# Kernel tuning notes

Measured on AMD Instinct MI355X. Metric: run time of the kernel, lower is better.

## Reference

```python
import jax, jax.numpy as jnp
import numpy as np

NEG_SLOPE = 0.2  # PyG GATv2Conv default negative_slope
EPS_BN = 1e-5


def gatv2(x, src, dst, ea, Wl, bl, Wr, br, We, att, bias, heads, C):
    """GATv2Conv (PyG semantics, eval mode / no dropout).
    x: [N, Fin]; src/dst: [Et] (self-loops already appended); ea: [Et, edge_dim].
    Returns (out [N, heads*C], alpha [Et, heads])."""
    N = x.shape[0]
    xl = (x @ Wl + bl).reshape(N, heads, C)   # lin_l -> source features
    xr = (x @ Wr + br).reshape(N, heads, C)   # lin_r -> target features
    e = (ea @ We).reshape(-1, heads, C)       # lin_edge (no bias in PyG)
    m = jax.nn.leaky_relu(xl[src] + xr[dst] + e, NEG_SLOPE)  # [Et, H, C]
    logit = jnp.einsum('ehc,hc->eh', m, att)                  # [Et, H]
    # segment softmax over destination node
    amax = jax.ops.segment_max(logit, dst, num_segments=N)
    expv = jnp.exp(logit - amax[dst])
    denom = jax.ops.segment_sum(expv, dst, num_segments=N)
    alpha = expv / (denom[dst] + 1e-16)
    out = jax.ops.segment_sum(xl[src] * alpha[:, :, None], dst, num_segments=N)
    return out.reshape(N, heads * C) + bias, alpha


def setup_inputs() -> dict:
    key = jax.random.key(0)
    ks = list(jax.random.split(key, 20))
    N, E, H, C = 100000, 1600000, 2, 32
    D = H * C  # 64
    def nrm(i, shape, s=0.1):
        return jax.random.normal(ks[i], shape, jnp.float32) * s
    return {
        'x': jax.random.normal(ks[0], (N, 2), jnp.float32),
        'edge_index': jax.random.randint(ks[1], (2, E), 0, N, dtype=jnp.int32),
        'edge_attr': jax.random.uniform(ks[2], (E, 1), dtype=jnp.float32),
        'Wl1': nrm(3, (2, D)), 'bl1': jnp.zeros((D,), jnp.float32),
        'Wr1': nrm(4, (2, D)), 'br1': jnp.zeros((D,), jnp.float32),
        'We1': nrm(5, (1, D)), 'att1': nrm(6, (H, C)), 'bias1': jnp.zeros((D,), jnp.float32),
        'skip_W': nrm(7, (2, D)), 'skip_b': jnp.zeros((D,), jnp.float32),
        'bn_gamma': jnp.ones((D,), jnp.float32), 'bn_beta': jnp.zeros((D,), jnp.float32),
        'Wl2': nrm(8, (D, C)), 'bl2': jnp.zeros((C,), jnp.float32),
        'Wr2': nrm(9, (D, C)), 'br2': jnp.zeros((C,), jnp.float32),
        'We2': nrm(10, (1, C)), 'att2': nrm(11, (1, C)), 'bias2': jnp.zeros((C,), jnp.float32),
        'Wc1': nrm(12, (C, C)), 'bc1': jnp.zeros((C,), jnp.float32),
        'Wc2': nrm(13, (C, 10)), 'bc2': jnp.zeros((10,), jnp.float32),
        'Wt1': nrm(14, (C, C)), 'bt1': jnp.zeros((C,), jnp.float32),
        'Wt2': nrm(15, (C, 20)), 'bt2': jnp.zeros((20,), jnp.float32),
    }


def reference(x, edge_index, edge_attr, Wl1, bl1, Wr1, br1, We1, att1, bias1,
              skip_W, skip_b, bn_gamma, bn_beta,
              Wl2, bl2, Wr2, br2, We2, att2, bias2,
              Wc1, bc1, Wc2, bc2, Wt1, bt1, Wt2, bt2):
    N = x.shape[0]
    src0, dst0 = edge_index[0], edge_index[1]
    # add_self_loops with fill_value='mean': self-loop attr = mean of incoming edge attrs per node
    loop = jnp.arange(N, dtype=edge_index.dtype)
    deg = jax.ops.segment_sum(jnp.ones(src0.shape, jnp.float32), dst0, num_segments=N)
    loop_attr = jax.ops.segment_sum(edge_attr, dst0, num_segments=N) / jnp.maximum(deg, 1.0)[:, None]
    src = jnp.concatenate([src0, loop])
    dst = jnp.concatenate([dst0, loop])
    ea = jnp.concatenate([edge_attr, loop_attr], axis=0)

    h, _ = gatv2(x, src, dst, ea, Wl1, bl1, Wr1, br1, We1, att1, bias1, heads=2, C=32)
    h = h + x @ skip_W + skip_b
    # BatchNorm1d, training-style batch statistics (deterministic)
    mu = h.mean(0)
    var = h.var(0)
    h = (h - mu) / jnp.sqrt(var + EPS_BN) * bn_gamma + bn_beta
    h = jax.nn.elu(h)
    h, alpha = gatv2(h, src, dst, ea, Wl2, bl2, Wr2, br2, We2, att2, bias2, heads=1, C=32)
    h = jax.nn.elu(h)
    h_type = jax.nn.relu(h @ Wt1 + bt1)
    h_clone = jax.nn.relu(h @ Wc1 + bc1)
    h_type = jax.nn.log_softmax(h_type @ Wt2 + bt2, axis=1)
    h_clone = jax.nn.log_softmax(h_clone @ Wc2 + bc2, axis=1)
    out = jnp.concatenate([h_clone, h_type], axis=1)  # [N, 30]
    return out, alpha
```

## Files before the change

### kernel.cpp

```cpp
#include <hip/hip_runtime.h>
#include <math.h>

#define NEG_SLOPE 0.2f
#define CNT_SHIFT 44
#define EA_SCALE 262144.0f
#define EA_INV (1.0f / 262144.0f)

typedef float f2 __attribute__((ext_vector_type(2)));
__device__ __forceinline__ f2 max2(f2 a, f2 b) { return __builtin_elementwise_max(a, b); }
__device__ __forceinline__ f2 lrelu2(f2 m) { return max2(m, m * NEG_SLOPE); }

__device__ __forceinline__ float lrelu(float x) { return fmaxf(x, NEG_SLOPE * x); }
__device__ __forceinline__ float elu1(float x) { return x > 0.f ? x : __expf(x) - 1.f; }

__global__ void k0p(const int* __restrict__ dst, const float* __restrict__ ea,
                    unsigned long long* __restrict__ packed,
                    unsigned short* __restrict__ rankA, int E) {
    int t = blockIdx.x * blockDim.x + threadIdx.x;
    if (t >= E) return;
    int d = dst[t];
    unsigned long long inc = (1ULL << CNT_SHIFT)
                           | (unsigned long long)__float2uint_rn(ea[t] * EA_SCALE);
    unsigned long long old = atomicAdd(&packed[d], inc);
    rankA[t] = (unsigned short)(old >> CNT_SHIFT);
}

__global__ void kscanA(const unsigned long long* __restrict__ packed,
                       int* __restrict__ rowstart, int* __restrict__ bsum,
                       int* __restrict__ cntA, float* __restrict__ asumA, int N) {
    __shared__ int sm[256];
    int t = threadIdx.x;
    int i = blockIdx.x * 256 + t;
    int v = 0;
    if (i < N) {
        unsigned long long p = packed[i];
        int c = (int)(p >> CNT_SHIFT);
        cntA[i] = c;
        asumA[i] = (float)(p & ((1ULL << CNT_SHIFT) - 1)) * EA_INV;
        v = c + 1;
    }
    sm[t] = v;
    __syncthreads();
    for (int off = 1; off < 256; off <<= 1) {
        int u = (t >= off) ? sm[t - off] : 0;
        __syncthreads();
        sm[t] += u;
        __syncthreads();
    }
    if (i < N) rowstart[i] = sm[t] - v;
    if (t == 255) bsum[blockIdx.x] = sm[255];
}

__global__ void kscanB(int* __restrict__ bsum, int B) {
    __shared__ int sm[512];
    int t = threadIdx.x;
    int v = (t < B) ? bsum[t] : 0;
    sm[t] = v;
    __syncthreads();
    for (int off = 1; off < 512; off <<= 1) {
        int u = (t >= off) ? sm[t - off] : 0;
        __syncthreads();
        sm[t] += u;
        __syncthreads();
    }
    if (t < B) bsum[t] = sm[t] - v;
}

__global__ void kscanC(int* __restrict__ rowstart, const int* __restrict__ bsum, int N) {
    int i = blockIdx.x * blockDim.x + threadIdx.x;
    if (i < N) rowstart[i] += bsum[i >> 8];
}

__global__ void kscatter(const int* __restrict__ srcA, const int* __restrict__ dstA,
                         const float* __restrict__ ea, const float* __restrict__ asumA,
                         const int* __restrict__ cntA, const int* __restrict__ rowstart,
                         const unsigned short* __restrict__ rankA,
                         int2* __restrict__ edge2, int* __restrict__ posA, int E, int Et) {
    int t = blockIdx.x * blockDim.x + threadIdx.x;
    if (t >= Et) return;
    if (t < E) {
        int d = dstA[t];
        int r = min((int)rankA[t], cntA[d] - 1);
        int pos = rowstart[d] + r;
        edge2[pos] = make_int2(srcA[t], __float_as_int(ea[t]));
        posA[t] = pos;
    } else {
        int d = t - E;
        int cd = cntA[d];
        int pos = rowstart[d] + cd;
        float eav = asumA[d] / fmaxf((float)cd, 1.0f);
        edge2[pos] = make_int2(d, __float_as_int(eav));
    }
}

__global__ void __launch_bounds__(256, 4)
kL1(const float* __restrict__ x, const int2* __restrict__ edge2,
    const int* __restrict__ rowst, const int* __restrict__ cntA,
    const float* __restrict__ Wl, const float* __restrict__ bl,
    const float* __restrict__ Wr, const float* __restrict__ br,
    const float* __restrict__ We, const float* __restrict__ att,
    float* __restrict__ dstat, int N) {
    int wid = blockIdx.x * 4 + (threadIdx.x >> 6);
    int TW = gridDim.x * 4;
    int lane = threadIdx.x & 63;
    int h = lane >> 5, lane5 = lane & 31;
    int slot = lane5 >> 3, cl = lane5 & 7;
    int dc = h * 32 + cl * 4;

    float4 t4;
    t4 = *(const float4*)(Wl + dc);        f2 wl0a = {t4.x, t4.y}, wl0b = {t4.z, t4.w};
    t4 = *(const float4*)(Wl + 64 + dc);   f2 wl1a = {t4.x, t4.y}, wl1b = {t4.z, t4.w};
    t4 = *(const float4*)(We + dc);        f2 weva = {t4.x, t4.y}, wevb = {t4.z, t4.w};
    t4 = *(const float4*)(att + dc);       f2 atva = {t4.x, t4.y}, atvb = {t4.z, t4.w};
    t4 = *(const float4*)(Wr + dc);        f2 wr0a = {t4.x, t4.y}, wr0b = {t4.z, t4.w};
    t4 = *(const float4*)(Wr + 64 + dc);   f2 wr1a = {t4.x, t4.y}, wr1b = {t4.z, t4.w};
    t4 = *(const float4*)(bl + dc);        f2 bba  = {t4.x, t4.y}, bbb  = {t4.z, t4.w};
    t4 = *(const float4*)(br + dc);        bba += (f2){t4.x, t4.y}; bbb += (f2){t4.z, t4.w};

    for (int n = wid; n < N; n += TW) {
        float2 xd = ((const float2*)x)[n];
        f2 dsta = bba + xd.x * wr0a + xd.y * wr1a;
        f2 dstb = bbb + xd.x * wr0b + xd.y * wr1b;
        int start = rowst[n], len = cntA[n] + 1;
        float pd = 0.f, pa = 0.f, pb = 0.f;
        for (int base = 0; base < len; base += 8) {
            int iA = base + slot, iB = base + 4 + slot;
            bool aA = iA < len, aB = iB < len;
            int2 eA = edge2[start + (aA ? iA : len - 1)];
            int2 eB = edge2[start + (aB ? iB : len - 1)];
            float2 xsA = ((const float2*)x)[eA.x];
            float2 xsB = ((const float2*)x)[eB.x];
            float evA = __int_as_float(eA.y), evB = __int_as_float(eB.y);
            f2 mAa = dsta + xsA.x * wl0a + xsA.y * wl1a + evA * weva;
            f2 mAb = dstb + xsA.x * wl0b + xsA.y * wl1b + evA * wevb;
            f2 mBa = dsta + xsB.x * wl0a + xsB.y * wl1a + evB * weva;
            f2 mBb = dstb + xsB.x * wl0b + xsB.y * wl1b + evB * wevb;
            f2 psA = lrelu2(mAa) * atva + lrelu2(mAb) * atvb;
            f2 psB = lrelu2(mBa) * atva + lrelu2(mBb) * atvb;
            float pA = psA.x + psA.y;
            float pB = psB.x + psB.y;
            pA += __shfl_xor(pA, 1); pB += __shfl_xor(pB, 1);
            pA += __shfl_xor(pA, 2); pB += __shfl_xor(pB, 2);
            pA += __shfl_xor(pA, 4); pB += __shfl_xor(pB, 4);
            float eevA = aA ? __expf(pA) : 0.f;
            float eevB = aB ? __expf(pB) : 0.f;
            pd += eevA + eevB;
            pa += eevA * xsA.x + eevB * xsB.x;
            pb += eevA * xsA.y + eevB * xsB.y;
        }
        pd += __shfl_xor(pd, 8);  pa += __shfl_xor(pa, 8);  pb += __shfl_xor(pb, 8);
        pd += __shfl_xor(pd, 16); pa += __shfl_xor(pa, 16); pb += __shfl_xor(pb, 16);
        if (lane5 == 0) {
            dstat[(size_t)n * 6 + h]     = pd;
            dstat[(size_t)n * 6 + 2 + h] = pa;
            dstat[(size_t)n * 6 + 4 + h] = pb;
        }
    }
}

__global__ void k3a(const float* __restrict__ x, const float* __restrict__ dstat,
                    const float* __restrict__ Wl, const float* __restrict__ bl,
                    const float* __restrict__ bias1,
                    const float* __restrict__ skW, const float* __restrict__ skb,
                    float* __restrict__ hout, float* __restrict__ partial, int N) {
    __shared__ float sv[256], sq[256];
    size_t total = (size_t)N * 64;
    size_t stride = (size_t)gridDim.x * blockDim.x;
    float s = 0.f, q = 0.f;
    for (size_t idx = (size_t)blockIdx.x * blockDim.x + threadIdx.x; idx < total; idx += stride) {
        int n = (int)(idx >> 6), d = (int)(idx & 63), h2 = d >> 5;
        const float* ps = &dstat[(size_t)n * 6];
        float den = ps[h2], t0 = ps[2 + h2], t1 = ps[4 + h2];
        float agg = t0 * Wl[d] + t1 * Wl[64 + d] + den * bl[d];
        float hv = agg / (den + 1e-16f) + bias1[d]
                 + x[2 * n] * skW[d] + x[2 * n + 1] * skW[64 + d] + skb[d];
        hout[idx] = hv;
        s += hv; q += hv * hv;
    }
    sv[threadIdx.x] = s; sq[threadIdx.x] = q;
    __syncthreads();
    if (threadIdx.x < 64) {
        float a = sv[threadIdx.x] + sv[threadIdx.x + 64] + sv[threadIdx.x + 128] + sv[threadIdx.x + 192];
        float b = sq[threadIdx.x] + sq[threadIdx.x + 64] + sq[threadIdx.x + 128] + sq[threadIdx.x + 192];
        partial[(size_t)blockIdx.x * 128 + threadIdx.x] = a;
        partial[(size_t)blockIdx.x * 128 + 64 + threadIdx.x] = b;
    }
}

__global__ void kred(const float* __restrict__ partial, float* __restrict__ mu,
                     float* __restrict__ rstd, int G, int N) {
    __shared__ float s1[256], s2[256];
    int c = blockIdx.x;
    float a = 0.f, b = 0.f;
    for (int i = threadIdx.x; i < G; i += blockDim.x) {
        a += partial[(size_t)i * 128 + c];
        b += partial[(size_t)i * 128 + 64 + c];
    }
    s1[threadIdx.x] = a; s2[threadIdx.x] = b;
    __syncthreads();
    for (int off = 128; off >= 1; off >>= 1) {
        if (threadIdx.x < off) {
            s1[threadIdx.x] += s1[threadIdx.x + off];
            s2[threadIdx.x] += s2[threadIdx.x + off];
        }
        __syncthreads();
    }
    if (threadIdx.x == 0) {
        float m = s1[0] / (float)N;
        float v = s2[0] / (float)N - m * m;
        mu[c] = m;
        rstd[c] = rsqrtf(v + 1e-5f);
    }
}

__global__ void k3c(const float* __restrict__ h, const float* __restrict__ mu,
                    const float* __restrict__ rstd, const float* __restrict__ gamma,
                    const float* __restrict__ beta,
                    const float* __restrict__ Wl, const float* __restrict__ bl,
                    const float* __restrict__ Wr, const float* __restrict__ br,
                    float* __restrict__ xl2, float* __restrict__ xr2, int N) {
    __shared__ float sh[4][64];
    int w = threadIdx.x >> 6, lane = threadIdx.x & 63;
    int n = blockIdx.x * 4 + w;
    bool valid = (n < N);
    if (valid) {
        float hv = h[(size_t)n * 64 + lane];
        hv = (hv - mu[lane]) * rstd[lane] * gamma[lane] + beta[lane];
        sh[w][lane] = elu1(hv);
    }
    __syncthreads();
    if (!valid) return;
    int c = lane & 31;
    const float* W = (lane < 32) ? Wl : Wr;
    const float* b = (lane < 32) ? bl : br;
    float acc = b[c];
    #pragma unroll
    for (int k = 0; k < 64; ++k) acc += sh[w][k] * W[k * 32 + c];
    ((lane < 32) ? xl2 : xr2)[(size_t)n * 32 + c] = acc;
}

__global__ void __launch_bounds__(256, 4)
kL2(const float* __restrict__ xl2, const float* __restrict__ xr2,
    const int2* __restrict__ edge2,
    const int* __restrict__ rowst, const int* __restrict__ cntA,
    const float* __restrict__ We, const float* __restrict__ att,
    float* __restrict__ evS, float* __restrict__ h2,
    float* __restrict__ denom2, int N) {
    int g = blockIdx.x * blockDim.x + threadIdx.x;
    int n = g >> 5;
    if (n >= N) return;
    int lane = g & 31;
    int slot = lane >> 3, cl = lane & 7;
    int c4 = cl * 4;
    float4 t4;
    t4 = *(const float4*)(We + c4);                      f2 weva = {t4.x, t4.y}, wevb = {t4.z, t4.w};
    t4 = *(const float4*)(att + c4);                     f2 atva = {t4.x, t4.y}, atvb = {t4.z, t4.w};
    t4 = *(const float4*)(xr2 + (size_t)n * 32 + c4);    f2 xrva = {t4.x, t4.y}, xrvb = {t4.z, t4.w};
    int start = rowst[n], len = cntA[n] + 1;
    float den = 0.f;
    f2 acca = {0.f, 0.f}, accb = {0.f, 0.f};

    for (int base = 0; base < len; base += 8) {
        int iA = base + slot, iB = base + 4 + slot;
        bool aA = iA < len, aB = iB < len;
        int2 eA = edge2[start + (aA ? iA : 0)];
        int2 eB = edge2[start + (aB ? iB : 0)];
        float4 xA4 = *(const float4*)(xl2 + (size_t)eA.x * 32 + c4);
        float4 xB4 = *(const float4*)(xl2 + (size_t)eB.x * 32 + c4);
        f2 xAa = {xA4.x, xA4.y}, xAb = {xA4.z, xA4.w};
        f2 xBa = {xB4.x, xB4.y}, xBb = {xB4.z, xB4.w};
        float evA = __int_as_float(eA.y), evB = __int_as_float(eB.y);
        f2 mAa = xAa + xrva + evA * weva;
        f2 mAb = xAb + xrvb + evA * wevb;
        f2 mBa = xBa + xrva + evB * weva;
        f2 mBb = xBb + xrvb + evB * wevb;
        f2 psA = lrelu2(mAa) * atva + lrelu2(mAb) * atvb;
        f2 psB = lrelu2(mBa) * atva + lrelu2(mBb) * atvb;
        float pA = psA.x + psA.y;
        float pB = psB.x + psB.y;
        pA += __shfl_xor(pA, 1); pB += __shfl_xor(pB, 1);
        pA += __shfl_xor(pA, 2); pB += __shfl_xor(pB, 2);
        pA += __shfl_xor(pA, 4); pB += __shfl_xor(pB, 4);
        float eevA = aA ? __expf(pA) : 0.f;
        float eevB = aB ? __expf(pB) : 0.f;
        if (cl == 0) {
            if (aA) evS[start + iA] = eevA;
            if (aB) evS[start + iB] = eevB;
        }
        den += eevA + eevB;
        acca += eevA * xAa + eevB * xBa;
        accb += eevA * xAb + eevB * xBb;
    }
    #pragma unroll
    for (int m = 8; m <= 16; m <<= 1) {
        den    += __shfl_xor(den, m);
        acca.x += __shfl_xor(acca.x, m);
        acca.y += __shfl_xor(acca.y, m);
        accb.x += __shfl_xor(accb.x, m);
        accb.y += __shfl_xor(accb.y, m);
    }
    float inv = 1.f / (den + 1e-16f);
    if (slot == 0) {
        float4 o = make_float4(acca.x * inv, acca.y * inv, accb.x * inv, accb.y * inv);
        *(float4*)(h2 + (size_t)n * 32 + c4) = o;
    }
    if (lane == 0) denom2[n] = den;
}

__global__ void k4c(const float* __restrict__ evS, const int* __restrict__ posA,
                    const int* __restrict__ dstA, const int* __restrict__ rowst,
                    const int* __restrict__ cntA, const float* __restrict__ denom,
                    float* __restrict__ alpha, int E, int Et) {
    int t = blockIdx.x * blockDim.x + threadIdx.x;
    if (t >= Et) return;
    float ev, den;
    if (t < E) {
        ev = evS[posA[t]];
        den = denom[dstA[t]];
    } else {
        int d = t - E;
        ev = evS[rowst[d] + cntA[d]];
        den = denom[d];
    }
    alpha[t] = ev / (den + 1e-16f);
}

__global__ void __launch_bounds__(256, 1)
k5(const float* __restrict__ h2, const float* __restrict__ bias2,
   const float* __restrict__ Wt1, const float* __restrict__ bt1,
   const float* __restrict__ Wt2, const float* __restrict__ bt2,
   const float* __restrict__ Wc1, const float* __restrict__ bc1,
   const float* __restrict__ Wc2, const float* __restrict__ bc2,
   float* __restrict__ out, int N) {
    __shared__ float sWt1[1024], sWc1[1024], sWt2[640], sWc2[320];
    __shared__ float sbt1[32], sbc1[32], sbt2[20], sbc2[10], sb2[32];
    for (int i = threadIdx.x; i < 1024; i += blockDim.x) { sWt1[i] = Wt1[i]; sWc1[i] = Wc1[i]; }
    for (int i = threadIdx.x; i < 640; i += blockDim.x) sWt2[i] = Wt2[i];
    for (int i = threadIdx.x; i < 320; i += blockDim.x) sWc2[i] = Wc2[i];
    if (threadIdx.x < 32) { sbt1[threadIdx.x] = bt1[threadIdx.x]; sbc1[threadIdx.x] = bc1[threadIdx.x]; sb2[threadIdx.x] = bias2[threadIdx.x]; }
    if (threadIdx.x < 20) sbt2[threadIdx.x] = bt2[threadIdx.x];
    if (threadIdx.x < 10) sbc2[threadIdx.x] = bc2[threadIdx.x];
    __syncthreads();
    int n = blockIdx.x * blockDim.x + threadIdx.x;
    if (n >= N) return;
    float h[32];
    #pragma unroll
    for (int k = 0; k < 32; ++k) h[k] = elu1(h2[(size_t)n * 32 + k] + sb2[k]);
    float lt[20], lc[10];
    #pragma unroll
    for (int o = 0; o < 20; ++o) lt[o] = sbt2[o];
    #pragma unroll
    for (int o = 0; o < 10; ++o) lc[o] = sbc2[o];
    #pragma unroll
    for (int j = 0; j < 32; ++j) {
        float at = sbt1[j], ac = sbc1[j];
        #pragma unroll
        for (int k = 0; k < 32; ++k) { at += h[k] * sWt1[k * 32 + j]; ac += h[k] * sWc1[k * 32 + j]; }
        float tj = fmaxf(at, 0.f), cj = fmaxf(ac, 0.f);
        #pragma unroll
        for (int o = 0; o < 20; ++o) lt[o] += tj * sWt2[j * 20 + o];
        #pragma unroll
        for (int o = 0; o < 10; ++o) lc[o] += cj * sWc2[j * 10 + o];
    }
    float mt = -1e30f, mc = -1e30f;
    #pragma unroll
    for (int o = 0; o < 20; ++o) mt = fmaxf(mt, lt[o]);
    #pragma unroll
    for (int o = 0; o < 10; ++o) mc = fmaxf(mc, lc[o]);
    float st = 0.f, sc = 0.f;
    #pragma unroll
    for (int o = 0; o < 20; ++o) st += __expf(lt[o] - mt);
    #pragma unroll
    for (int o = 0; o < 10; ++o) sc += __expf(lc[o] - mc);
    float lset = mt + __logf(st);
    float lsec = mc + __logf(sc);
    #pragma unroll
    for (int o = 0; o < 10; ++o) out[(size_t)n * 30 + o] = lc[o] - lsec;
    #pragma unroll
    for (int o = 0; o < 20; ++o) out[(size_t)n * 30 + 10 + o] = lt[o] - lset;
}

extern "C" void kernel_launch(void* const* d_in, const int* in_sizes, int n_in,
                              void* d_out, int out_size, void* d_ws, size_t ws_size,
                              hipStream_t stream) {
    const float* x     = (const float*)d_in[0];
    const int*   ei    = (const int*)d_in[1];
    const float* eattr = (const float*)d_in[2];
    const float* Wl1   = (const float*)d_in[3];
    const float* bl1   = (const float*)d_in[4];
    const float* Wr1   = (const float*)d_in[5];
    const float* br1   = (const float*)d_in[6];
    const float* We1   = (const float*)d_in[7];
    const float* att1  = (const float*)d_in[8];
    const float* bias1 = (const float*)d_in[9];
    const float* skW   = (const float*)d_in[10];
    const float* skb   = (const float*)d_in[11];
    const float* gamma = (const float*)d_in[12];
    const float* beta  = (const float*)d_in[13];
    const float* Wl2   = (const float*)d_in[14];
    const float* bl2   = (const float*)d_in[15];
    const float* Wr2   = (const float*)d_in[16];
    const float* br2   = (const float*)d_in[17];
    const float* We2   = (const float*)d_in[18];
    const float* att2  = (const float*)d_in[19];
    const float* bias2 = (const float*)d_in[20];
    const float* Wc1   = (const float*)d_in[21];
    const float* bc1   = (const float*)d_in[22];
    const float* Wc2   = (const float*)d_in[23];
    const float* bc2   = (const float*)d_in[24];
    const float* Wt1   = (const float*)d_in[25];
    const float* bt1   = (const float*)d_in[26];
    const float* Wt2   = (const float*)d_in[27];
    const float* bt2   = (const float*)d_in[28];

    const int N  = in_sizes[0] / 2;
    const int E  = in_sizes[1] / 2;
    const int Et = E + N;
    const int* srcA = ei;
    const int* dstA = ei + E;
    const int G3 = 1024;
    const int B  = (N + 255) / 256;

    char* p = (char*)d_ws;
    unsigned long long* packed = (unsigned long long*)p; p += (size_t)N * 8;
    int2*  edge2  = (int2*)p;  p += (size_t)Et * 8;
    int*   posA   = (int*)p;   p += (size_t)E * 4;
    unsigned short* rankA = (unsigned short*)p; p += (size_t)E * 2;
    float* hbuf   = (float*)p; p += (size_t)N * 64 * 4;
    float* xl2    = (float*)p; p += (size_t)N * 32 * 4;
    float* xr2    = (float*)p; p += (size_t)N * 32 * 4;
    float* evS    = (float*)p; p += (size_t)Et * 4;
    float* dstat  = (float*)p; p += (size_t)N * 6 * 4;
    int*   cntA   = (int*)p;   p += (size_t)N * 4;
    float* asumA  = (float*)p; p += (size_t)N * 4;
    int*   rowst  = (int*)p;   p += (size_t)N * 4;
    int*   bsum   = (int*)p;   p += 512 * 4;
    float* partial= (float*)p; p += (size_t)G3 * 128 * 4;
    float* mu     = (float*)p; p += 64 * 4;
    float* rstd   = (float*)p; p += 64 * 4;
    float* denom2 = (float*)p; p += (size_t)N * 4;
    float* h2     = hbuf;

    float* outMain  = (float*)d_out;
    float* outAlpha = outMain + (size_t)N * 30;

    hipMemsetAsync(packed, 0, (size_t)N * 8, stream);
    k0p<<<(E + 255) / 256, 256, 0, stream>>>(dstA, eattr, packed, rankA, E);
    kscanA<<<B, 256, 0, stream>>>(packed, rowst, bsum, cntA, asumA, N);
    kscanB<<<1, 512, 0, stream>>>(bsum, B);
    kscanC<<<B, 256, 0, stream>>>(rowst, bsum, N);
    kscatter<<<(Et + 255) / 256, 256, 0, stream>>>(srcA, dstA, eattr, asumA, cntA,
                                                   rowst, rankA, edge2, posA, E, Et);

    kL1<<<2048, 256, 0, stream>>>(x, edge2, rowst, cntA,
                                  Wl1, bl1, Wr1, br1, We1, att1, dstat, N);

    k3a<<<G3, 256, 0, stream>>>(x, dstat, Wl1, bl1, bias1, skW, skb, hbuf, partial, N);
    kred<<<64, 256, 0, stream>>>(partial, mu, rstd, G3, N);
    k3c<<<(N + 3) / 4, 256, 0, stream>>>(hbuf, mu, rstd, gamma, beta,
                                         Wl2, bl2, Wr2, br2, xl2, xr2, N);

    kL2<<<((size_t)N * 32 + 255) / 256, 256, 0, stream>>>(xl2, xr2, edge2, rowst, cntA,
                                                          We2, att2, evS, h2, denom2, N);
    k4c<<<(Et + 255) / 256, 256, 0, stream>>>(evS, posA, dstA, rowst, cntA, denom2,
                                              outAlpha, E, Et);

    k5<<<(N + 255) / 256, 256, 0, stream>>>(h2, bias2, Wt1, bt1, Wt2, bt2,
                                            Wc1, bc1, Wc2, bc2, outMain, N);
    (void)n_in; (void)out_size; (void)ws_size;
}
```

Before: 361.0 us.

## Compute layer-1 attention exps per edge in original order, scatter into CSR records

Layer-1 edge logits and their exponentials are now computed in the counting kernel, one thread per edge in coalesced original order, with no max subtraction, matching the old code. The results are scattered alongside the src/ea pair into a wider 32-byte CSR record. kL1 becomes a simple reduction over contiguous records, removing the random x gathers and the per-edge compute inside the per-node loop. The cost is a 4x larger edge record (more scatter bytes and a strided read in kL2), a per-edge 64-channel serial loop, and an evq buffer that overlaps hbuf.

```diff
diff --git a/kernel.cpp b/kernel.cpp
--- a/kernel.cpp
+++ b/kernel.cpp
@@ -13,16 +13,47 @@
 __device__ __forceinline__ float lrelu(float x) { return fmaxf(x, NEG_SLOPE * x); }
 __device__ __forceinline__ float elu1(float x) { return x > 0.f ? x : __expf(x) - 1.f; }
 
-__global__ void k0p(const int* __restrict__ dst, const float* __restrict__ ea,
+
+__global__ void k0p(const int* __restrict__ srcA, const int* __restrict__ dstA,
+                    const float* __restrict__ ea, const float* __restrict__ x,
+                    const float* __restrict__ Wl, const float* __restrict__ bl,
+                    const float* __restrict__ Wr, const float* __restrict__ br,
+                    const float* __restrict__ We, const float* __restrict__ att,
                     unsigned long long* __restrict__ packed,
-                    unsigned short* __restrict__ rankA, int E) {
+                    unsigned short* __restrict__ rankA,
+                    float4* __restrict__ evq, int E) {
+    __shared__ float sW[7][64];
+    if (threadIdx.x < 64) {
+        int d = threadIdx.x;
+        sW[0][d] = Wl[d];  sW[1][d] = Wl[64 + d];
+        sW[2][d] = We[d];  sW[3][d] = att[d];
+        sW[4][d] = Wr[d];  sW[5][d] = Wr[64 + d];
+        sW[6][d] = bl[d] + br[d];
+    }
+    __syncthreads();
     int t = blockIdx.x * blockDim.x + threadIdx.x;
     if (t >= E) return;
-    int d = dst[t];
+    int d = dstA[t], s = srcA[t];
+    float eav = ea[t];
     unsigned long long inc = (1ULL << CNT_SHIFT)
-                           | (unsigned long long)__float2uint_rn(ea[t] * EA_SCALE);
+                           | (unsigned long long)__float2uint_rn(eav * EA_SCALE);
     unsigned long long old = atomicAdd(&packed[d], inc);
     rankA[t] = (unsigned short)(old >> CNT_SHIFT);
+
+    float2 xs = ((const float2*)x)[s];
+    float2 xd = ((const float2*)x)[d];
+    float l0 = 0.f, l1 = 0.f;
+    #pragma unroll
+    for (int c = 0; c < 32; ++c) {
+        float m0 = xd.x * sW[4][c] + xd.y * sW[5][c] + sW[6][c]
+                 + xs.x * sW[0][c] + xs.y * sW[1][c] + eav * sW[2][c];
+        l0 += lrelu(m0) * sW[3][c];
+        int c2 = c + 32;
+        float m1 = xd.x * sW[4][c2] + xd.y * sW[5][c2] + sW[6][c2]
+                 + xs.x * sW[0][c2] + xs.y * sW[1][c2] + eav * sW[2][c2];
+        l1 += lrelu(m1) * sW[3][c2];
+    }
+    evq[t] = make_float4(__expf(l0), __expf(l1), xs.x, xs.y);
 }
 
 __global__ void kscanA(const unsigned long long* __restrict__ packed,
@@ -72,89 +103,82 @@
 }
 
 __global__ void kscatter(const int* __restrict__ srcA, const int* __restrict__ dstA,
-                         const float* __restrict__ ea, const float* __restrict__ asumA,
+                         const float* __restrict__ ea, const float* __restrict__ x,
+                         const float* __restrict__ asumA,
                          const int* __restrict__ cntA, const int* __restrict__ rowstart,
                          const unsigned short* __restrict__ rankA,
-                         int2* __restrict__ edge2, int* __restrict__ posA, int E, int Et) {
+                         const float4* __restrict__ evq,
+                         const float* __restrict__ Wl, const float* __restrict__ bl,
+                         const float* __restrict__ Wr, const float* __restrict__ br,
+                         const float* __restrict__ We, const float* __restrict__ att,
+                         int2* __restrict__ rec, int* __restrict__ posA, int E, int Et) {
+    __shared__ float sW[7][64];
+    if (threadIdx.x < 64) {
+        int d = threadIdx.x;
+        sW[0][d] = Wl[d];  sW[1][d] = Wl[64 + d];
+        sW[2][d] = We[d];  sW[3][d] = att[d];
+        sW[4][d] = Wr[d];  sW[5][d] = Wr[64 + d];
+        sW[6][d] = bl[d] + br[d];
+    }
+    __syncthreads();
     int t = blockIdx.x * blockDim.x + threadIdx.x;
     if (t >= Et) return;
     if (t < E) {
         int d = dstA[t];
         int r = min((int)rankA[t], cntA[d] - 1);
         int pos = rowstart[d] + r;
-        edge2[pos] = make_int2(srcA[t], __float_as_int(ea[t]));
+        rec[(size_t)pos * 4]     = make_int2(srcA[t], __float_as_int(ea[t]));
+        ((float4*)rec)[(size_t)pos * 2 + 1] = evq[t];
         posA[t] = pos;
     } else {
         int d = t - E;
         int cd = cntA[d];
         int pos = rowstart[d] + cd;
         float eav = asumA[d] / fmaxf((float)cd, 1.0f);
-        edge2[pos] = make_int2(d, __float_as_int(eav));
-    }
-}
-
-__global__ void __launch_bounds__(256, 4)
-kL1(const float* __restrict__ x, const int2* __restrict__ edge2,
-    const int* __restrict__ rowst, const int* __restrict__ cntA,
-    const float* __restrict__ Wl, const float* __restrict__ bl,
-    const float* __restrict__ Wr, const float* __restrict__ br,
-    const float* __restrict__ We, const float* __restrict__ att,
-    float* __restrict__ dstat, int N) {
-    int wid = blockIdx.x * 4 + (threadIdx.x >> 6);
-    int TW = gridDim.x * 4;
-    int lane = threadIdx.x & 63;
-    int h = lane >> 5, lane5 = lane & 31;
-    int slot = lane5 >> 3, cl = lane5 & 7;
-    int dc = h * 32 + cl * 4;
-
-    float4 t4;
-    t4 = *(const float4*)(Wl + dc);        f2 wl0a = {t4.x, t4.y}, wl0b = {t4.z, t4.w};
-    t4 = *(const float4*)(Wl + 64 + dc);   f2 wl1a = {t4.x, t4.y}, wl1b = {t4.z, t4.w};
-    t4 = *(const float4*)(We + dc);        f2 weva = {t4.x, t4.y}, wevb = {t4.z, t4.w};
-    t4 = *(const float4*)(att + dc);       f2 atva = {t4.x, t4.y}, atvb = {t4.z, t4.w};
-    t4 = *(const float4*)(Wr + dc);        f2 wr0a = {t4.x, t4.y}, wr0b = {t4.z, t4.w};
-    t4 = *(const float4*)(Wr + 64 + dc);   f2 wr1a = {t4.x, t4.y}, wr1b = {t4.z, t4.w};
-    t4 = *(const float4*)(bl + dc);        f2 bba  = {t4.x, t4.y}, bbb  = {t4.z, t4.w};
-    t4 = *(const float4*)(br + dc);        bba += (f2){t4.x, t4.y}; bbb += (f2){t4.z, t4.w};
-
-    for (int n = wid; n < N; n += TW) {
-        float2 xd = ((const float2*)x)[n];
-        f2 dsta = bba + xd.x * wr0a + xd.y * wr1a;
-        f2 dstb = bbb + xd.x * wr0b + xd.y * wr1b;
-        int start = rowst[n], len = cntA[n] + 1;
-        float pd = 0.f, pa = 0.f, pb = 0.f;
-        for (int base = 0; base < len; base += 8) {
-            int iA = base + slot, iB = base + 4 + slot;
-            bool aA = iA < len, aB = iB < len;
-            int2 eA = edge2[start + (aA ? iA : len - 1)];
-            int2 eB = edge2[start + (aB ? iB : len - 1)];
-            float2 xsA = ((const float2*)x)[eA.x];
-            float2 xsB = ((const float2*)x)[eB.x];
-            float evA = __int_as_float(eA.y), evB = __int_as_float(eB.y);
-            f2 mAa = dsta + xsA.x * wl0a + xsA.y * wl1a + evA * weva;
-            f2 mAb = dstb + xsA.x * wl0b + xsA.y * wl1b + evA * wevb;
-            f2 mBa = dsta + xsB.x * wl0a + xsB.y * wl1a + evB * weva;
-            f2 mBb = dstb + xsB.x * wl0b + xsB.y * wl1b + evB * wevb;
-            f2 psA = lrelu2(mAa) * atva + lrelu2(mAb) * atvb;
-            f2 psB = lrelu2(mBa) * atva + lrelu2(mBb) * atvb;
-            float pA = psA.x + psA.y;
-            float pB = psB.x + psB.y;
-            pA += __shfl_xor(pA, 1); pB += __shfl_xor(pB, 1);
-            pA += __shfl_xor(pA, 2); pB += __shfl_xor(pB, 2);
-            pA += __shfl_xor(pA, 4); pB += __shfl_xor(pB, 4);
-            float eevA = aA ? __expf(pA) : 0.f;
-            float eevB = aB ? __expf(pB) : 0.f;
-            pd += eevA + eevB;
-            pa += eevA * xsA.x + eevB * xsB.x;
-            pb += eevA * xsA.y + eevB * xsB.y;
+        float2 xd = ((const float2*)x)[d];
+        float l0 = 0.f, l1 = 0.f;
+        #pragma unroll
+        for (int c = 0; c < 32; ++c) {
+            float m0 = xd.x * (sW[4][c] + sW[0][c]) + xd.y * (sW[5][c] + sW[1][c])
+                     + sW[6][c] + eav * sW[2][c];
+            l0 += lrelu(m0) * sW[3][c];
+            int c2 = c + 32;
+            float m1 = xd.x * (sW[4][c2] + sW[0][c2]) + xd.y * (sW[5][c2] + sW[1][c2])
+                     + sW[6][c2] + eav * sW[2][c2];
+            l1 += lrelu(m1) * sW[3][c2];
         }
-        pd += __shfl_xor(pd, 8);  pa += __shfl_xor(pa, 8);  pb += __shfl_xor(pb, 8);
-        pd += __shfl_xor(pd, 16); pa += __shfl_xor(pa, 16); pb += __shfl_xor(pb, 16);
-        if (lane5 == 0) {
-            dstat[(size_t)n * 6 + h]     = pd;
-            dstat[(size_t)n * 6 + 2 + h] = pa;
-            dstat[(size_t)n * 6 + 4 + h] = pb;
-        }
+        rec[(size_t)pos * 4]     = make_int2(d, __float_as_int(eav));
+        ((float4*)rec)[(size_t)pos * 2 + 1] =
+            make_float4(__expf(l0), __expf(l1), xd.x, xd.y);
+    }
+}
+
+__global__ void kL1(const int2* __restrict__ rec,
+                    const int* __restrict__ rowst, const int* __restrict__ cntA,
+                    float* __restrict__ dstat, int N) {
+    int g = threadIdx.x >> 4, l16 = threadIdx.x & 15;
+    int n = blockIdx.x * 16 + g;
+    if (n >= N) return;
+    int start = rowst[n], len = cntA[n] + 1;
+    const float4* recq = (const float4*)rec;
+    float pd0 = 0.f, pd1 = 0.f, pa0 = 0.f, pa1 = 0.f, pb0 = 0.f, pb1 = 0.f;
+    for (int i = l16; i < len; i += 16) {
+        float4 q = recq[(size_t)(start + i) * 2 + 1];
+        pd0 += q.x;        pd1 += q.y;
+        pa0 += q.x * q.z;  pa1 += q.y * q.z;
+        pb0 += q.x * q.w;  pb1 += q.y * q.w;
+    }
+    #pragma unroll
+    for (int m = 1; m < 16; m <<= 1) {
+        pd0 += __shfl_xor(pd0, m); pd1 += __shfl_xor(pd1, m);
+        pa0 += __shfl_xor(pa0, m); pa1 += __shfl_xor(pa1, m);
+        pb0 += __shfl_xor(pb0, m); pb1 += __shfl_xor(pb1, m);
+    }
+    if (l16 == 0) {
+        float* ps = &dstat[(size_t)n * 6];
+        ps[0] = pd0; ps[1] = pd1;
+        ps[2] = pa0; ps[3] = pa1;
+        ps[4] = pb0; ps[5] = pb1;
     }
 }
 
@@ -241,7 +265,7 @@
 
 __global__ void __launch_bounds__(256, 4)
 kL2(const float* __restrict__ xl2, const float* __restrict__ xr2,
-    const int2* __restrict__ edge2,
+    const int2* __restrict__ rec,
     const int* __restrict__ rowst, const int* __restrict__ cntA,
     const float* __restrict__ We, const float* __restrict__ att,
     float* __restrict__ evS, float* __restrict__ h2,
@@ -263,8 +287,8 @@
     for (int base = 0; base < len; base += 8) {
         int iA = base + slot, iB = base + 4 + slot;
         bool aA = iA < len, aB = iB < len;
-        int2 eA = edge2[start + (aA ? iA : 0)];
-        int2 eB = edge2[start + (aB ? iB : 0)];
+        int2 eA = rec[(size_t)(start + (aA ? iA : 0)) * 4];
+        int2 eB = rec[(size_t)(start + (aB ? iB : 0)) * 4];
         float4 xA4 = *(const float4*)(xl2 + (size_t)eA.x * 32 + c4);
         float4 xB4 = *(const float4*)(xl2 + (size_t)eB.x * 32 + c4);
         f2 xAa = {xA4.x, xA4.y}, xAb = {xA4.z, xA4.w};
@@ -423,10 +447,14 @@
 
     char* p = (char*)d_ws;
     unsigned long long* packed = (unsigned long long*)p; p += (size_t)N * 8;
-    int2*  edge2  = (int2*)p;  p += (size_t)Et * 8;
+    int2*  rec    = (int2*)p;  p += (size_t)Et * 32;
     int*   posA   = (int*)p;   p += (size_t)E * 4;
     unsigned short* rankA = (unsigned short*)p; p += (size_t)E * 2;
-    float* hbuf   = (float*)p; p += (size_t)N * 64 * 4;
+    size_t hbytes = (size_t)N * 64 * 4;
+    size_t ebytes = (size_t)E * 16;
+    size_t ovl = hbytes > ebytes ? hbytes : ebytes;
+    float4* evq   = (float4*)p;
+    float*  hbuf  = (float*)p; p += ovl;
     float* xl2    = (float*)p; p += (size_t)N * 32 * 4;
     float* xr2    = (float*)p; p += (size_t)N * 32 * 4;
     float* evS    = (float*)p; p += (size_t)Et * 4;
@@ -445,22 +473,25 @@
     float* outAlpha = outMain + (size_t)N * 30;
 
     hipMemsetAsync(packed, 0, (size_t)N * 8, stream);
-    k0p<<<(E + 255) / 256, 256, 0, stream>>>(dstA, eattr, packed, rankA, E);
+    k0p<<<(E + 255) / 256, 256, 0, stream>>>(srcA, dstA, eattr, x,
+                                             Wl1, bl1, Wr1, br1, We1, att1,
+                                             packed, rankA, evq, E);
     kscanA<<<B, 256, 0, stream>>>(packed, rowst, bsum, cntA, asumA, N);
     kscanB<<<1, 512, 0, stream>>>(bsum, B);
     kscanC<<<B, 256, 0, stream>>>(rowst, bsum, N);
-    kscatter<<<(Et + 255) / 256, 256, 0, stream>>>(srcA, dstA, eattr, asumA, cntA,
-                                                   rowst, rankA, edge2, posA, E, Et);
-
-    kL1<<<2048, 256, 0, stream>>>(x, edge2, rowst, cntA,
-                                  Wl1, bl1, Wr1, br1, We1, att1, dstat, N);
+    kscatter<<<(Et + 255) / 256, 256, 0, stream>>>(srcA, dstA, eattr, x, asumA, cntA,
+                                                   rowst, rankA, evq,
+                                                   Wl1, bl1, Wr1, br1, We1, att1,
+                                                   rec, posA, E, Et);
+
+    kL1<<<(N + 15) / 16, 256, 0, stream>>>(rec, rowst, cntA, dstat, N);
 
     k3a<<<G3, 256, 0, stream>>>(x, dstat, Wl1, bl1, bias1, skW, skb, hbuf, partial, N);
     kred<<<64, 256, 0, stream>>>(partial, mu, rstd, G3, N);
     k3c<<<(N + 3) / 4, 256, 0, stream>>>(hbuf, mu, rstd, gamma, beta,
                                          Wl2, bl2, Wr2, br2, xl2, xr2, N);
 
-    kL2<<<((size_t)N * 32 + 255) / 256, 256, 0, stream>>>(xl2, xr2, edge2, rowst, cntA,
+    kL2<<<((size_t)N * 32 + 255) / 256, 256, 0, stream>>>(xl2, xr2, rec, rowst, cntA,
                                                           We2, att2, evS, h2, denom2, N);
     k4c<<<(Et + 255) / 256, 256, 0, stream>>>(evS, posA, dstA, rowst, cntA, denom2,
                                               outAlpha, E, Et);
```

New measurement: 324.9 us. 1.11x faster.
